# Kernel optimization log

Measured on AMD Instinct MI355X. Metric: run time of the kernel, lower is better.

## Reference

```python
import jax, jax.numpy as jnp
import numpy as np

N_HEADS = 16
HEAD_SIZE = 64
EMBED = 1024
BLOCK = 2048
B, T = 2, 2048


def setup_inputs() -> dict:
    key = jax.random.key(0)
    ks = jax.random.split(key, 6)
    scale = 0.02
    inputs = jax.random.normal(ks[0], (B, T, EMBED), dtype=jnp.float32)
    # per-head projection weights, stacked: [H, E, D]
    Wk = jax.random.normal(ks[1], (N_HEADS, EMBED, HEAD_SIZE), dtype=jnp.float32) * scale
    Wq = jax.random.normal(ks[2], (N_HEADS, EMBED, HEAD_SIZE), dtype=jnp.float32) * scale
    Wv = jax.random.normal(ks[3], (N_HEADS, EMBED, HEAD_SIZE), dtype=jnp.float32) * scale
    Wo = jax.random.normal(ks[4], (EMBED, EMBED), dtype=jnp.float32) * scale
    bo = jax.random.normal(ks[5], (EMBED,), dtype=jnp.float32) * scale
    return {"inputs": inputs, "Wk": Wk, "Wq": Wq, "Wv": Wv, "Wo": Wo, "bo": bo}


def reference(inputs, Wk, Wq, Wv, Wo, bo):
    # per-head projections: [B,H,T,D]
    k = jnp.einsum("bte,hed->bhtd", inputs, Wk)
    q = jnp.einsum("bte,hed->bhtd", inputs, Wq)
    v = jnp.einsum("bte,hed->bhtd", inputs, Wv)
    # NOTE: original computes wei = K @ Q^T (faithful reproduction)
    wei = jnp.einsum("bhtd,bhsd->bhts", k, q) * (HEAD_SIZE ** -0.5)
    causal = jnp.tril(jnp.ones((T, T), dtype=bool))  # tril==0 masked
    wei = jnp.where(causal, wei, -jnp.inf)
    wei = jax.nn.softmax(wei, axis=-1)
    out = jnp.einsum("bhts,bhsd->bhtd", wei, v)
    # concat heads along feature dim: [B,T,H*D]
    z = out.transpose(0, 2, 1, 3).reshape(B, T, N_HEADS * HEAD_SIZE)
    z = z @ Wo.T + bo  # match torch Linear(x) = x @ W^T + b
    return z
```

## Files before the change

kernel.cpp:

```cpp
#include <hip/hip_runtime.h>
#include <cstdint>
#include <cstddef>

typedef __bf16 bf8_t __attribute__((ext_vector_type(8)));
typedef float  f4_t  __attribute__((ext_vector_type(4)));
typedef unsigned u32x2_t __attribute__((ext_vector_type(2)));

static __device__ __forceinline__ f4_t mfma16(bf8_t a, bf8_t b, f4_t c) {
    return __builtin_amdgcn_mfma_f32_16x16x32_bf16(a, b, c, 0, 0, 0);
}

#if defined(__has_builtin) && __has_builtin(__builtin_amdgcn_exp2f)
#define EXP2F(x) __builtin_amdgcn_exp2f(x)
#else
#define EXP2F(x) exp2f(x)
#endif

static __device__ __forceinline__ void plane32swap(unsigned& a, unsigned& b) {
#if defined(__has_builtin) && __has_builtin(__builtin_amdgcn_permlane32_swap)
    u32x2_t r = __builtin_amdgcn_permlane32_swap(a, b, false, false);
    a = r[0]; b = r[1];
#else
    unsigned ax = __shfl_xor(a, 32);
    unsigned bx = __shfl_xor(b, 32);
    bool hi = ((threadIdx.x & 63) >= 32);
    unsigned na = hi ? bx : a;
    unsigned nb = hi ? b : ax;
    a = na; b = nb;
#endif
}

static __device__ __forceinline__ unsigned pack2(float a, float b) {
    __bf16 lo = (__bf16)a, hi = (__bf16)b;
    unsigned short ulo = __builtin_bit_cast(unsigned short, lo);
    unsigned short uhi = __builtin_bit_cast(unsigned short, hi);
    return (unsigned)ulo | ((unsigned)uhi << 16);
}

static __device__ __forceinline__ void async_ld16(const __bf16* g, __bf16* l) {
    __builtin_amdgcn_global_load_lds(
        (const __attribute__((address_space(1))) void*)(uintptr_t)g,
        (__attribute__((address_space(3))) void*)(uintptr_t)l, 16, 0, 0);
}


__global__ void __launch_bounds__(256) prep_all(const float* __restrict__ X,
                                                const float* __restrict__ Wo,
                                                const float* __restrict__ Wq,
                                                const float* __restrict__ Wk,
                                                const float* __restrict__ Wv,
                                                __bf16* __restrict__ Xbf,
                                                __bf16* __restrict__ Wobf,
                                                __bf16* __restrict__ Wqt,
                                                __bf16* __restrict__ Wkt,
                                                __bf16* __restrict__ Wvt,
                                                int* __restrict__ ctrs) {
    __shared__ float tile[64][65];
    int bx = (int)blockIdx.x;
    if (bx == 0 && threadIdx.x < 128) ctrs[threadIdx.x] = 0;
    if (bx < 2560) {
        const float* src; __bf16* dst; size_t base;
        if (bx < 2048) { src = X;  dst = Xbf;  base = (size_t)bx * 2048; }
        else           { src = Wo; dst = Wobf; base = (size_t)(bx - 2048) * 2048; }
        size_t i = base + (size_t)threadIdx.x * 8;
        float4 a = *(const float4*)(src + i);
        float4 b = *(const float4*)(src + i + 4);
        bf8_t o;
        o[0] = (__bf16)a.x; o[1] = (__bf16)a.y; o[2] = (__bf16)a.z; o[3] = (__bf16)a.w;
        o[4] = (__bf16)b.x; o[5] = (__bf16)b.y; o[6] = (__bf16)b.z; o[7] = (__bf16)b.w;
        *(bf8_t*)(dst + i) = o;
        return;
    }
    int wt = bx - 2560;
    int which = wt >> 8, inner = wt & 255;
    const float* W; __bf16* Wt;
    if (which == 0)      { W = Wq; Wt = Wqt; }
    else if (which == 1) { W = Wk; Wt = Wkt; }
    else                 { W = Wv; Wt = Wvt; }
    int h = inner >> 4, eb = inner & 15;
    int tx = threadIdx.x;
    int e = tx >> 2, dg = (tx & 3) * 16;
    const float* src = W + ((size_t)h * 1024 + eb * 64 + e) * 64 + dg;
#pragma unroll
    for (int i = 0; i < 4; ++i) {
        float4 v = *(const float4*)(src + i * 4);
        tile[dg + i * 4 + 0][e] = v.x;
        tile[dg + i * 4 + 1][e] = v.y;
        tile[dg + i * 4 + 2][e] = v.z;
        tile[dg + i * 4 + 3][e] = v.w;
    }
    __syncthreads();
    int d = tx >> 2, eg = (tx & 3) * 16;
    __bf16* dst = Wt + (size_t)(h * 64 + d) * 1024 + eb * 64 + eg;
    bf8_t o0, o1;
#pragma unroll
    for (int i = 0; i < 8; ++i) o0[i] = (__bf16)tile[d][eg + i];
#pragma unroll
    for (int i = 0; i < 8; ++i) o1[i] = (__bf16)tile[d][eg + 8 + i];
    *(bf8_t*)dst       = o0;
    *(bf8_t*)(dst + 8) = o1;
}

static __device__ __forceinline__ void gemm_tile128(const __bf16* __restrict__ A,
                                                    const __bf16* __restrict__ Bt,
                                                    __bf16* As, __bf16* Bs,
                                                    int m0, int n0, f4_t acc[4][4]) {
    const int tid  = threadIdx.x;
    const int lane = tid & 63;
    const int wv   = tid >> 6;
    const int lrow = lane >> 3;
    const int lsc  = lane & 7;
    const int quad = lane >> 4;
    const int l15  = lane & 15;
    const int wm = (wv & 1) * 64;
    const int wn = (wv >> 1) * 64;
    f4_t zero = {0.f, 0.f, 0.f, 0.f};
#pragma unroll
    for (int mi = 0; mi < 4; ++mi)
#pragma unroll
        for (int ni = 0; ni < 4; ++ni) acc[mi][ni] = zero;

    for (int kb = 0; kb < 16; ++kb) {
#pragma unroll
        for (int j = 0; j < 4; ++j) {
            int row = wv * 32 + j * 8 + lrow;
            int lc  = lsc ^ (row & 7);
            async_ld16(A + (size_t)(m0 + row) * 1024 + kb * 64 + lc * 8,
                       As + (wv * 32 + j * 8) * 64);
            async_ld16(Bt + (size_t)(n0 + row) * 1024 + kb * 64 + lc * 8,
                       Bs + (wv * 32 + j * 8) * 64);
        }
        __syncthreads();
#pragma unroll
        for (int ks = 0; ks < 2; ++ks) {
            bf8_t af[4], bfr[4];
#pragma unroll
            for (int mi = 0; mi < 4; ++mi) {
                int row = wm + mi * 16 + l15;
                int ch  = (ks * 4 + quad) ^ (row & 7);
                af[mi] = *(const bf8_t*)(As + row * 64 + ch * 8);
            }
#pragma unroll
            for (int ni = 0; ni < 4; ++ni) {
                int row = wn + ni * 16 + l15;
                int ch  = (ks * 4 + quad) ^ (row & 7);
                bfr[ni] = *(const bf8_t*)(Bs + row * 64 + ch * 8);
            }
#pragma unroll
            for (int mi = 0; mi < 4; ++mi)
#pragma unroll
                for (int ni = 0; ni < 4; ++ni)
                    acc[mi][ni] = mfma16(af[mi], bfr[ni], acc[mi][ni]);
        }
        __syncthreads();
    }
}

__global__ void __launch_bounds__(256, 3) gemm_proj(const __bf16* __restrict__ Xbf,
                                                    const __bf16* __restrict__ Wqt,
                                                    const __bf16* __restrict__ Wkt,
                                                    const __bf16* __restrict__ Wvt,
                                                    __bf16* __restrict__ Qb,
                                                    __bf16* __restrict__ Kb,
                                                    __bf16* __restrict__ Vt) {
    __shared__ __bf16 smem[17408];
    __bf16* As = smem;
    __bf16* Bs = smem + 8192;
    int which = blockIdx.y;
    const __bf16* Bt = which == 0 ? Wqt : (which == 1 ? Wkt : Wvt);
    int bx = (int)blockIdx.x;
    int xcd = bx & 7, qq = bx >> 3;
    int m0 = (xcd * 4 + (qq & 3)) * 128;
    int n0 = (qq >> 2) * 128;
    f4_t acc[4][4];
    gemm_tile128(Xbf, Bt, As, Bs, m0, n0, acc);
    const int lane = threadIdx.x & 63, wv = threadIdx.x >> 6;
    const int quad = lane >> 4, l15 = lane & 15;
    const int wm = (wv & 1) * 64, wn = (wv >> 1) * 64;
    const int STR = 136;
    if (which < 2) {
        __bf16* C = which ? Kb : Qb;
        const float scl = which ? 0.18033688f : 1.0f;
#pragma unroll
        for (int mi = 0; mi < 4; ++mi)
#pragma unroll
            for (int ni = 0; ni < 4; ++ni)
#pragma unroll
                for (int r = 0; r < 4; ++r) {
                    int ml = wm + mi * 16 + quad * 4 + r;
                    int nl = wn + ni * 16 + l15;
                    smem[ml * STR + nl] = (__bf16)(acc[mi][ni][r] * scl);
                }
        __syncthreads();
        int row = (int)threadIdx.x >> 1;
        int seg = (int)threadIdx.x & 1;
        int m = m0 + row;
        int b = m >> 11, t = m & 2047;
        int h = (n0 >> 6) + seg;
        __bf16* dst = C + ((size_t)(b * 16 + h) * 2048 + t) * 64;
        const __bf16* srcl = smem + row * STR + seg * 64;
#pragma unroll
        for (int k = 0; k < 8; ++k)
            *(bf8_t*)(dst + k * 8) = *(const bf8_t*)(srcl + k * 8);
    } else {
#pragma unroll
        for (int mi = 0; mi < 4; ++mi)
#pragma unroll
            for (int ni = 0; ni < 4; ++ni)
#pragma unroll
                for (int r = 0; r < 4; ++r) {
                    int ml = wm + mi * 16 + quad * 4 + r;
                    int nl = wn + ni * 16 + l15;
                    smem[nl * STR + ml] = (__bf16)acc[mi][ni][r];
                }
        __syncthreads();
        int b = m0 >> 11, tg0 = m0 & 2047;
        int nl = (int)threadIdx.x >> 1;
        int tc = ((int)threadIdx.x & 1) * 64;
        int n = n0 + nl, h = n >> 6, d = n & 63;
        __bf16* dst = Vt + ((size_t)(b * 16 + h) * 64 + d) * 2048 + tg0 + tc;
        const __bf16* srcl = smem + nl * STR + tc;
#pragma unroll
        for (int k = 0; k < 8; ++k)
            *(bf8_t*)(dst + k * 8) = *(const bf8_t*)(srcl + k * 8);
    }
}

static __device__ __forceinline__ void gemm_tile(const __bf16* __restrict__ A,
                                                 const __bf16* __restrict__ Bt,
                                                 __bf16* As, __bf16* Bs,
                                                 int m0, int n0, f4_t acc[4][2]) {
    const int tid  = threadIdx.x;
    const int lane = tid & 63;
    const int wv   = tid >> 6;
    const int lrow = lane >> 3;
    const int lsc  = lane & 7;
    const int quad = lane >> 4;
    const int l15  = lane & 15;
    const int wm = (wv & 1) * 64;
    const int wn = (wv >> 1) * 32;
    f4_t zero = {0.f, 0.f, 0.f, 0.f};
#pragma unroll
    for (int mi = 0; mi < 4; ++mi)
#pragma unroll
        for (int ni = 0; ni < 2; ++ni) acc[mi][ni] = zero;

    for (int kb = 0; kb < 16; ++kb) {
#pragma unroll
        for (int j = 0; j < 4; ++j) {
            int row = wv * 32 + j * 8 + lrow;
            int lc  = lsc ^ (row & 7);
            async_ld16(A + (size_t)(m0 + row) * 1024 + kb * 64 + lc * 8,
                       As + (wv * 32 + j * 8) * 64);
        }
#pragma unroll
        for (int j = 0; j < 2; ++j) {
            int row = wv * 16 + j * 8 + lrow;
            int lc  = lsc ^ (row & 7);
            async_ld16(Bt + (size_t)(n0 + row) * 1024 + kb * 64 + lc * 8,
                       Bs + (wv * 16 + j * 8) * 64);
        }
        __syncthreads();
#pragma unroll
        for (int ks = 0; ks < 2; ++ks) {
            bf8_t af[4], bfr[2];
#pragma unroll
            for (int mi = 0; mi < 4; ++mi) {
                int row = wm + mi * 16 + l15;
                int ch  = (ks * 4 + quad) ^ (row & 7);
                af[mi] = *(const bf8_t*)(As + row * 64 + ch * 8);
            }
#pragma unroll
            for (int ni = 0; ni < 2; ++ni) {
                int row = wn + ni * 16 + l15;
                int ch  = (ks * 4 + quad) ^ (row & 7);
                bfr[ni] = *(const bf8_t*)(Bs + row * 64 + ch * 8);
            }
#pragma unroll
            for (int mi = 0; mi < 4; ++mi)
#pragma unroll
                for (int ni = 0; ni < 2; ++ni)
                    acc[mi][ni] = mfma16(af[mi], bfr[ni], acc[mi][ni]);
        }
        __syncthreads();
    }
}

__global__ void __launch_bounds__(256) gemm_out(const __bf16* __restrict__ Ob,
                                                const __bf16* __restrict__ Wobf,
                                                const float* __restrict__ bo,
                                                float* __restrict__ out) {
    __shared__ __bf16 smem[128 * 64 + 64 * 64];
    __bf16* As = smem;
    __bf16* Bs = smem + 128 * 64;
    int bx = (int)blockIdx.x;
    int xcd = bx & 7, qq = bx >> 3;
    int m0 = (xcd * 4 + (qq & 3)) * 128;
    int n0 = (qq >> 2) * 64;
    f4_t acc[4][2];
    gemm_tile(Ob, Wobf, As, Bs, m0, n0, acc);
    const int lane = threadIdx.x & 63, wv = threadIdx.x >> 6;
    const int quad = lane >> 4, l15 = lane & 15;
    const int wm = (wv & 1) * 64, wn = (wv >> 1) * 32;
#pragma unroll
    for (int mi = 0; mi < 4; ++mi)
#pragma unroll
        for (int ni = 0; ni < 2; ++ni)
#pragma unroll
            for (int r = 0; r < 4; ++r) {
                int m = m0 + wm + mi * 16 + quad * 4 + r;
                int n = n0 + wn + ni * 16 + l15;
                out[(size_t)m * 1024 + n] = acc[mi][ni][r] + bo[n];
            }
}

__global__ void __launch_bounds__(256, 4) attn(const __bf16* __restrict__ Kb,
                                               const __bf16* __restrict__ Qb,
                                               const __bf16* __restrict__ Vt,
                                               __bf16* __restrict__ Ob,
                                               int* __restrict__ ctrs) {
    __shared__ __bf16 Qs[2][64 * 64];
    __shared__ __bf16 Vs[2][64 * 64];
    __shared__ int item_lds;
    const int tid = threadIdx.x, lane = tid & 63, wv = tid >> 6;
    const int quad = lane >> 4, l15 = lane & 15;
    const int lrow8 = lane >> 3, lchunk = lane & 7;
    const bool qodd = (quad & 1) != 0;
    int xcc;
    asm volatile("s_getreg_b32 %0, hwreg(HW_REG_XCC_ID)" : "=s"(xcc));
    xcc &= 7;
    int* ctr = ctrs + xcc * 16;
    f4_t zero = {0.f, 0.f, 0.f, 0.f};

    for (;;) {
        if (tid == 0) item_lds = atomicAdd(ctr, 1);
        __syncthreads();
        const int q = item_lds;
        if (q >= 128) break;
        const int tt = 31 - (q >> 2);
        const int bh = xcc * 4 + (q & 3);
        const int b = bh >> 4, h = bh & 15;
        const int t0 = tt * 64;
        const int tw = t0 + wv * 16;
        const __bf16* Kp = Kb + (size_t)bh * 2048 * 64;
        const __bf16* Qp = Qb + (size_t)bh * 2048 * 64;
        const __bf16* Vp = Vt + (size_t)bh * 64 * 2048;

        bf8_t kfrag[2];
#pragma unroll
        for (int ks = 0; ks < 2; ++ks)
            kfrag[ks] = *(const bf8_t*)(Kp + (size_t)(tw + l15) * 64 + ks * 32 + quad * 8);

        f4_t oacc[4];
#pragma unroll
        for (int ni = 0; ni < 4; ++ni) oacc[ni] = zero;
        float lsum = 0.f;

        auto stage = [&](int buf, int s0) {
#pragma unroll
            for (int j = 0; j < 2; ++j) {
                int row = wv * 8 + j * 32 + lrow8;
                int cg  = lchunk ^ (row & 7);
                async_ld16(Qp + (size_t)(s0 + row) * 64 + cg * 8,
                           &Qs[buf][(wv * 8 + j * 32) * 64]);
                async_ld16(Vp + (size_t)row * 2048 + s0 + cg * 8,
                           &Vs[buf][(wv * 8 + j * 32) * 64]);
            }
        };

        const int nsb = tt + 1;
        stage(0, 0);
        for (int sb = 0; sb < nsb; ++sb) {
            const int cur = sb & 1;
            const int s0 = sb * 64;
            const bool masked = (sb == nsb - 1);
            __syncthreads();
            if (sb + 1 < nsb) stage(1 ^ cur, s0 + 64);
            const __bf16* Qc = &Qs[cur][0];
            const __bf16* Vc = &Vs[cur][0];
            f4_t sacc[4] = {zero, zero, zero, zero};
            __builtin_amdgcn_s_setprio(1);
#pragma unroll
            for (int ks = 0; ks < 2; ++ks) {
                bf8_t qf[4];
#pragma unroll
                for (int st = 0; st < 4; ++st) {
                    int row = st * 16 + l15;
                    int ch  = (ks * 4 + quad) ^ (row & 7);
                    qf[st] = *(const bf8_t*)(Qc + row * 64 + ch * 8);
                }
#pragma unroll
                for (int st = 0; st < 4; ++st)
                    sacc[st] = mfma16(qf[st], kfrag[ks], sacc[st]);
            }
            __builtin_amdgcn_s_setprio(0);
            const int lim = tw + l15 - s0;
#pragma unroll
            for (int st = 0; st < 4; ++st)
#pragma unroll
                for (int r = 0; r < 4; ++r) {
                    float e = EXP2F(sacc[st][r]);
                    if (masked && (st * 16 + quad * 4 + r > lim)) e = 0.0f;
                    lsum += e;
                    sacc[st][r] = e;
                }
            unsigned pk[4][2];
#pragma unroll
            for (int st = 0; st < 4; ++st)
#pragma unroll
                for (int rp = 0; rp < 2; ++rp)
                    pk[st][rp] = pack2(sacc[st][2 * rp], sacc[st][2 * rp + 1]);
            bf8_t pf[2];
#pragma unroll
            for (int ks = 0; ks < 2; ++ks) {
                unsigned w0, w1, w2, w3;
                {
                    unsigned A = pk[2 * ks][0], B = pk[2 * ks + 1][0];
                    plane32swap(A, B);
                    unsigned As_ = __shfl_xor(A, 16);
                    unsigned Bs_ = __shfl_xor(B, 16);
                    w0 = qodd ? Bs_ : A;
                    w2 = qodd ? B : As_;
                }
                {
                    unsigned A = pk[2 * ks][1], B = pk[2 * ks + 1][1];
                    plane32swap(A, B);
                    unsigned As_ = __shfl_xor(A, 16);
                    unsigned Bs_ = __shfl_xor(B, 16);
                    w1 = qodd ? Bs_ : A;
                    w3 = qodd ? B : As_;
                }
                union { unsigned u[4]; bf8_t v; } cv;
                cv.u[0] = w0; cv.u[1] = w1; cv.u[2] = w2; cv.u[3] = w3;
                pf[ks] = cv.v;
            }
            __builtin_amdgcn_s_setprio(1);
#pragma unroll
            for (int ks = 0; ks < 2; ++ks) {
                bf8_t vf[4];
#pragma unroll
                for (int ni = 0; ni < 4; ++ni) {
                    int row = ni * 16 + l15;
                    int ch  = (ks * 4 + quad) ^ (row & 7);
                    vf[ni] = *(const bf8_t*)(Vc + row * 64 + ch * 8);
                }
#pragma unroll
                for (int ni = 0; ni < 4; ++ni)
                    oacc[ni] = mfma16(pf[ks], vf[ni], oacc[ni]);
            }
            __builtin_amdgcn_s_setprio(0);
        }

        float l = lsum;
        l += __shfl_xor(l, 16);
        l += __shfl_xor(l, 32);
        float inv = 1.0f / l;
#pragma unroll
        for (int r = 0; r < 4; ++r) {
            float invr = __shfl(inv, quad * 4 + r);
            int t = tw + quad * 4 + r;
#pragma unroll
            for (int ni = 0; ni < 4; ++ni)
                Ob[((size_t)(b * 2048 + t) * 16 + h) * 64 + ni * 16 + l15] =
                    (__bf16)(oacc[ni][r] * invr);
        }
    }
}

extern "C" void kernel_launch(void* const* d_in, const int* in_sizes, int n_in,
                              void* d_out, int out_size, void* d_ws, size_t ws_size,
                              hipStream_t stream) {
    const float* X  = (const float*)d_in[0];
    const float* Wk = (const float*)d_in[1];
    const float* Wq = (const float*)d_in[2];
    const float* Wv = (const float*)d_in[3];
    const float* Wo = (const float*)d_in[4];
    const float* bo = (const float*)d_in[5];
    float* out = (float*)d_out;

    __bf16* ws   = (__bf16*)d_ws;
    __bf16* Xbf  = ws;
    __bf16* Wqt  = ws + 4194304;
    __bf16* Wkt  = ws + 5242880;
    __bf16* Wvt  = ws + 6291456;
    __bf16* Wobf = ws + 7340032;
    __bf16* Qb   = ws + 8388608;
    __bf16* Kb   = ws + 12582912;
    __bf16* Vt   = ws + 16777216;
    __bf16* Ob   = ws + 20971520;
    int* ctrs = (int*)out;

    prep_all<<<3328, 256, 0, stream>>>(X, Wo, Wq, Wk, Wv, Xbf, Wobf, Wqt, Wkt, Wvt, ctrs);
    gemm_proj<<<dim3(256, 3), 256, 0, stream>>>(Xbf, Wqt, Wkt, Wvt, Qb, Kb, Vt);
    attn<<<768, 256, 0, stream>>>(Kb, Qb, Vt, Ob, ctrs);
    gemm_out<<<512, 256, 0, stream>>>(Ob, Wobf, bo, out);
}
```

Measured before the change: 169.6 us.

## Load Q and V fragments directly from global memory instead of LDS staging

```diff
diff --git a/kernel.cpp b/kernel.cpp
--- a/kernel.cpp
+++ b/kernel.cpp
@@ -319,12 +319,9 @@
                                                const __bf16* __restrict__ Vt,
                                                __bf16* __restrict__ Ob,
                                                int* __restrict__ ctrs) {
-    __shared__ __bf16 Qs[2][64 * 64];
-    __shared__ __bf16 Vs[2][64 * 64];
     __shared__ int item_lds;
     const int tid = threadIdx.x, lane = tid & 63, wv = tid >> 6;
     const int quad = lane >> 4, l15 = lane & 15;
-    const int lrow8 = lane >> 3, lchunk = lane & 7;
     const bool qodd = (quad & 1) != 0;
     int xcc;
     asm volatile("s_getreg_b32 %0, hwreg(HW_REG_XCC_ID)" : "=s"(xcc));
@@ -336,6 +333,7 @@
         if (tid == 0) item_lds = atomicAdd(ctr, 1);
         __syncthreads();
         const int q = item_lds;
+        __syncthreads();
         if (q >= 128) break;
         const int tt = 31 - (q >> 2);
         const int bh = xcc * 4 + (q & 3);
@@ -356,44 +354,31 @@
         for (int ni = 0; ni < 4; ++ni) oacc[ni] = zero;
         float lsum = 0.f;
 
-        auto stage = [&](int buf, int s0) {
-#pragma unroll
-            for (int j = 0; j < 2; ++j) {
-                int row = wv * 8 + j * 32 + lrow8;
-                int cg  = lchunk ^ (row & 7);
-                async_ld16(Qp + (size_t)(s0 + row) * 64 + cg * 8,
-                           &Qs[buf][(wv * 8 + j * 32) * 64]);
-                async_ld16(Vp + (size_t)row * 2048 + s0 + cg * 8,
-                           &Vs[buf][(wv * 8 + j * 32) * 64]);
-            }
-        };
-
         const int nsb = tt + 1;
-        stage(0, 0);
         for (int sb = 0; sb < nsb; ++sb) {
-            const int cur = sb & 1;
             const int s0 = sb * 64;
             const bool masked = (sb == nsb - 1);
-            __syncthreads();
-            if (sb + 1 < nsb) stage(1 ^ cur, s0 + 64);
-            const __bf16* Qc = &Qs[cur][0];
-            const __bf16* Vc = &Vs[cur][0];
+            bf8_t vf[2][4];
+#pragma unroll
+            for (int ks = 0; ks < 2; ++ks)
+#pragma unroll
+                for (int ni = 0; ni < 4; ++ni)
+                    vf[ks][ni] = *(const bf8_t*)(Vp + (size_t)(ni * 16 + l15) * 2048 +
+                                                 s0 + ks * 32 + quad * 8);
             f4_t sacc[4] = {zero, zero, zero, zero};
-            __builtin_amdgcn_s_setprio(1);
 #pragma unroll
             for (int ks = 0; ks < 2; ++ks) {
                 bf8_t qf[4];
 #pragma unroll
-                for (int st = 0; st < 4; ++st) {
-                    int row = st * 16 + l15;
-                    int ch  = (ks * 4 + quad) ^ (row & 7);
-                    qf[st] = *(const bf8_t*)(Qc + row * 64 + ch * 8);
-                }
+                for (int st = 0; st < 4; ++st)
+                    qf[st] = *(const bf8_t*)(Qp + (size_t)(s0 + st * 16 + l15) * 64 +
+                                             ks * 32 + quad * 8);
+                __builtin_amdgcn_s_setprio(1);
 #pragma unroll
                 for (int st = 0; st < 4; ++st)
                     sacc[st] = mfma16(qf[st], kfrag[ks], sacc[st]);
-            }
-            __builtin_amdgcn_s_setprio(0);
+                __builtin_amdgcn_s_setprio(0);
+            }
             const int lim = tw + l15 - s0;
 #pragma unroll
             for (int st = 0; st < 4; ++st)
@@ -436,18 +421,10 @@
             }
             __builtin_amdgcn_s_setprio(1);
 #pragma unroll
-            for (int ks = 0; ks < 2; ++ks) {
-                bf8_t vf[4];
-#pragma unroll
-                for (int ni = 0; ni < 4; ++ni) {
-                    int row = ni * 16 + l15;
-                    int ch  = (ks * 4 + quad) ^ (row & 7);
-                    vf[ni] = *(const bf8_t*)(Vc + row * 64 + ch * 8);
-                }
+            for (int ks = 0; ks < 2; ++ks)
 #pragma unroll
                 for (int ni = 0; ni < 4; ++ni)
-                    oacc[ni] = mfma16(pf[ks], vf[ni], oacc[ni]);
-            }
+                    oacc[ni] = mfma16(pf[ks], vf[ks][ni], oacc[ni]);
             __builtin_amdgcn_s_setprio(0);
         }
 
```

Result: slower. 263.2 us (+55.2%).

## Split long causal attention rows across two work items and merge partials

Applied to the files above, without the earlier changes.

```diff
diff --git a/kernel.cpp b/kernel.cpp
--- a/kernel.cpp
+++ b/kernel.cpp
@@ -314,10 +314,24 @@
             }
 }
 
+__device__ const unsigned char ITEMS[48] = {
+    124, 125, 121, 62,
+    120, 116, 117, 113, 58,
+    112, 108, 109, 105, 54,
+    104, 100, 101, 97, 50,
+    96, 92, 93, 89, 46,
+    88, 84, 85, 81, 42,
+    80, 76, 77, 73, 38,
+    72, 68, 69, 65, 34,
+    64, 30,
+    26, 22, 18, 14, 10, 6, 2
+};
 __global__ void __launch_bounds__(256, 4) attn(const __bf16* __restrict__ Kb,
                                                const __bf16* __restrict__ Qb,
                                                const __bf16* __restrict__ Vt,
                                                __bf16* __restrict__ Ob,
+                                               __bf16* __restrict__ Opart,
+                                               float* __restrict__ Lpart,
                                                int* __restrict__ ctrs) {
     __shared__ __bf16 Qs[2][64 * 64];
     __shared__ __bf16 Vs[2][64 * 64];
@@ -336,12 +350,16 @@
         if (tid == 0) item_lds = atomicAdd(ctr, 1);
         __syncthreads();
         const int q = item_lds;
-        if (q >= 128) break;
-        const int tt = 31 - (q >> 2);
+        if (q >= 192) break;
+        const int code = ITEMS[q >> 2];
+        const int tt = code >> 2, c = code & 3;
         const int bh = xcc * 4 + (q & 3);
         const int b = bh >> 4, h = bh & 15;
         const int t0 = tt * 64;
         const int tw = t0 + wv * 16;
+        const int sMid = (tt + 1) >> 1;
+        const int sLo = (c == 1) ? sMid : 0;
+        const int sHi = (c == 0) ? sMid : tt + 1;
         const __bf16* Kp = Kb + (size_t)bh * 2048 * 64;
         const __bf16* Qp = Qb + (size_t)bh * 2048 * 64;
         const __bf16* Vp = Vt + (size_t)bh * 64 * 2048;
@@ -368,14 +386,13 @@
             }
         };
 
-        const int nsb = tt + 1;
-        stage(0, 0);
-        for (int sb = 0; sb < nsb; ++sb) {
+        stage(sLo & 1, sLo * 64);
+        for (int sb = sLo; sb < sHi; ++sb) {
             const int cur = sb & 1;
             const int s0 = sb * 64;
-            const bool masked = (sb == nsb - 1);
+            const bool masked = (sb == tt);
             __syncthreads();
-            if (sb + 1 < nsb) stage(1 ^ cur, s0 + 64);
+            if (sb + 1 < sHi) stage(1 ^ cur, s0 + 64);
             const __bf16* Qc = &Qs[cur][0];
             const __bf16* Vc = &Vs[cur][0];
             f4_t sacc[4] = {zero, zero, zero, zero};
@@ -454,17 +471,50 @@
         float l = lsum;
         l += __shfl_xor(l, 16);
         l += __shfl_xor(l, 32);
-        float inv = 1.0f / l;
-#pragma unroll
-        for (int r = 0; r < 4; ++r) {
-            float invr = __shfl(inv, quad * 4 + r);
-            int t = tw + quad * 4 + r;
-#pragma unroll
-            for (int ni = 0; ni < 4; ++ni)
-                Ob[((size_t)(b * 2048 + t) * 16 + h) * 64 + ni * 16 + l15] =
-                    (__bf16)(oacc[ni][r] * invr);
+        if (c != 2) {
+            if (quad == 0)
+                Lpart[c * 32768 + bh * 1024 + (tw - 1024) + l15] = l;
+            size_t pb = (size_t)(c * 32 + bh) * 1024 + (tw - 1024);
+#pragma unroll
+            for (int r = 0; r < 4; ++r)
+#pragma unroll
+                for (int ni = 0; ni < 4; ++ni)
+                    Opart[(pb + quad * 4 + r) * 64 + ni * 16 + l15] =
+                        (__bf16)oacc[ni][r];
+        } else {
+            float inv = 1.0f / l;
+#pragma unroll
+            for (int r = 0; r < 4; ++r) {
+                float invr = __shfl(inv, quad * 4 + r);
+                int t = tw + quad * 4 + r;
+#pragma unroll
+                for (int ni = 0; ni < 4; ++ni)
+                    Ob[((size_t)(b * 2048 + t) * 16 + h) * 64 + ni * 16 + l15] =
+                        (__bf16)(oacc[ni][r] * invr);
+            }
         }
     }
+}
+
+__global__ void __launch_bounds__(256) attn_merge(const __bf16* __restrict__ Opart,
+                                                  const float* __restrict__ Lpart,
+                                                  __bf16* __restrict__ Ob) {
+    int gid = (int)blockIdx.x * 256 + (int)threadIdx.x;
+    int bh = gid >> 13;
+    int rem = gid & 8191;
+    int tl = rem >> 3;
+    int dg = (rem & 7) * 8;
+    float l0 = Lpart[bh * 1024 + tl];
+    float l1 = Lpart[32768 + bh * 1024 + tl];
+    float inv = 1.0f / (l0 + l1);
+    bf8_t a = *(const bf8_t*)(Opart + ((size_t)bh * 1024 + tl) * 64 + dg);
+    bf8_t c = *(const bf8_t*)(Opart + ((size_t)(32 + bh) * 1024 + tl) * 64 + dg);
+    bf8_t o;
+#pragma unroll
+    for (int i = 0; i < 8; ++i)
+        o[i] = (__bf16)(((float)a[i] + (float)c[i]) * inv);
+    int b = bh >> 4, h = bh & 15, t = 1024 + tl;
+    *(bf8_t*)(Ob + ((size_t)(b * 2048 + t) * 16 + h) * 64 + dg) = o;
 }
 
 extern "C" void kernel_launch(void* const* d_in, const int* in_sizes, int n_in,
@@ -488,10 +538,13 @@
     __bf16* Kb   = ws + 12582912;
     __bf16* Vt   = ws + 16777216;
     __bf16* Ob   = ws + 20971520;
+    float*  Lpart = (float*)(ws + 1048576);
+    __bf16* Opart = ws + 2097152;
     int* ctrs = (int*)out;
 
     prep_all<<<3328, 256, 0, stream>>>(X, Wo, Wq, Wk, Wv, Xbf, Wobf, Wqt, Wkt, Wvt, ctrs);
     gemm_proj<<<dim3(256, 3), 256, 0, stream>>>(Xbf, Wqt, Wkt, Wvt, Qb, Kb, Vt);
-    attn<<<768, 256, 0, stream>>>(Kb, Qb, Vt, Ob, ctrs);
+    attn<<<768, 256, 0, stream>>>(Kb, Qb, Vt, Ob, Opart, Lpart, ctrs);
+    attn_merge<<<1024, 256, 0, stream>>>(Opart, Lpart, Ob);
     gemm_out<<<512, 256, 0, stream>>>(Ob, Wobf, bo, out);
 }
```

New measurement: 173.3 us. 2.2% more time.
